# Optimization experiments

Measured on AMD Instinct MI355X. Metric: run time of the kernel, lower is better.

Reference implementation:

```python
import jax, jax.numpy as jnp
import numpy as np

HIDDEN = 1152
N_HEADS = 4
N_KV = 1
HEAD_DIM = 256
EPS = 1e-6
B, S = 4, 2048
ROPE_THETA = 1000000.0


def _rms_norm(x, w):
    # x: [..., D] float32; Gemma-style (1 + w) scale
    xf = x.astype(jnp.float32)
    inv = jax.lax.rsqrt(jnp.mean(xf * xf, axis=-1, keepdims=True) + EPS)
    return (xf * inv * (1.0 + w.astype(jnp.float32))).astype(x.dtype)


def _apply_rope(x, cos, sin):
    # x: [B, H, S, D]; cos/sin: [S, D/2]
    d2 = x.shape[-1] // 2
    x1, x2 = x[..., :d2], x[..., d2:]
    cos = cos[None, None, :, :]
    sin = sin[None, None, :, :]
    xr = x1 * cos - x2 * sin
    xi = x1 * sin + x2 * cos
    return jnp.concatenate([xr, xi], axis=-1).astype(x.dtype)


def setup_inputs() -> dict:
    key = jax.random.key(0)
    k_h, k_qkv, k_qn, k_kn, k_o = jax.random.split(key, 5)
    hidden_states = jax.random.normal(k_h, (B, S, HIDDEN), dtype=jnp.float32)
    # causal additive mask [1,1,S,S]
    neg = jnp.finfo(jnp.float32).min
    causal = jnp.tril(jnp.ones((S, S), dtype=bool))
    attention_mask = jnp.where(causal, 0.0, neg)[None, None, :, :].astype(jnp.float32)
    # RoPE tables (complex freqs_cis split into cos/sin)
    inv_freq = 1.0 / (ROPE_THETA ** (np.arange(0, HEAD_DIM, 2, dtype=np.float32) / HEAD_DIM))
    ang = np.arange(S, dtype=np.float32)[:, None] * inv_freq[None, :]
    freqs_cos = jnp.asarray(np.cos(ang))
    freqs_sin = jnp.asarray(np.sin(ang))
    qkv_out = (N_HEADS + 2 * N_KV) * HEAD_DIM
    scale = HIDDEN ** -0.5
    w_qkv = jax.random.normal(k_qkv, (HIDDEN, qkv_out), dtype=jnp.float32) * scale
    w_o = jax.random.normal(k_o, (N_HEADS * HEAD_DIM, HIDDEN), dtype=jnp.float32) * (N_HEADS * HEAD_DIM) ** -0.5
    q_norm_w = jax.random.normal(k_qn, (HEAD_DIM,), dtype=jnp.float32) * 0.02
    k_norm_w = jax.random.normal(k_kn, (HEAD_DIM,), dtype=jnp.float32) * 0.02
    return {
        "hidden_states": hidden_states,
        "attention_mask": attention_mask,
        "freqs_cos": freqs_cos,
        "freqs_sin": freqs_sin,
        "w_qkv": w_qkv,
        "q_norm_w": q_norm_w,
        "k_norm_w": k_norm_w,
        "w_o": w_o,
    }


def reference(hidden_states, attention_mask, freqs_cos, freqs_sin, w_qkv, q_norm_w, k_norm_w, w_o):
    b, s, _ = hidden_states.shape
    groups = N_HEADS // N_KV
    scaling = HEAD_DIM ** -0.5

    qkv = jnp.einsum("bsh,ho->bso", hidden_states, w_qkv)
    q_end = N_HEADS * HEAD_DIM
    k_end = q_end + N_KV * HEAD_DIM
    q = qkv[:, :, :q_end].reshape(b, s, N_HEADS, HEAD_DIM).transpose(0, 2, 1, 3)
    k = qkv[:, :, q_end:k_end].reshape(b, s, N_KV, HEAD_DIM).transpose(0, 2, 1, 3)
    v = qkv[:, :, k_end:].reshape(b, s, N_KV, HEAD_DIM).transpose(0, 2, 1, 3)

    q = _rms_norm(q, q_norm_w)
    k = _rms_norm(k, k_norm_w)

    q = _apply_rope(q, freqs_cos, freqs_sin)
    k = _apply_rope(k, freqs_cos, freqs_sin)

    if groups > 1:
        k = jnp.repeat(k, groups, axis=1)  # [B, H, S, D]
        v = jnp.repeat(v, groups, axis=1)

    scores = jnp.einsum("bhqd,bhkd->bhqk", q * scaling, k)
    scores = scores + attention_mask.astype(jnp.float32)
    probs = jax.nn.softmax(scores.astype(jnp.float32), axis=-1).astype(q.dtype)

    attn = jnp.einsum("bhqk,bhkd->bhqd", probs, v)
    attn = attn.transpose(0, 2, 1, 3).reshape(b, s, N_HEADS * HEAD_DIM)
    return jnp.einsum("bsf,fh->bsh", attn, w_o)
```

## Files before the change

kernel.cpp:

```cpp
#include <hip/hip_runtime.h>

typedef _Float16 f16;
typedef _Float16 f16x8 __attribute__((ext_vector_type(8)));
typedef _Float16 f16x4 __attribute__((ext_vector_type(4)));
typedef float f32x4 __attribute__((ext_vector_type(4)));

#define NH 4
#define HD 256
#define BB 4
#define SS 2048
#define HID 1152
#define QKV_N 1536
#define ODIM (NH * HD)

#define QKV16_OFF 0L
#define OBUF_OFF 0L
#define OPART_OFF 16777216L
#define ML_OFF 44040192L
#define QB_OFF 50331648L
#define KB_OFF 67108864L
#define VT_OFF 71303168L
#define WQKVT_OFF 75497472L
#define WOT_OFF 79036416L

#define GLL16(gp, lp)                                                      \
  __builtin_amdgcn_global_load_lds(                                       \
      (const __attribute__((address_space(1))) char*)(gp),                \
      (__attribute__((address_space(3))) char*)(lp), 16, 0, 0)

template <typename ST>
__global__ __launch_bounds__(256) void transpose_cvt(
    const ST* __restrict__ src, long src_ld, long src_bs,
    f16* __restrict__ dst, long dst_ld, long dst_bs) {
  __shared__ float tile[32][33];
  src += (long)blockIdx.z * src_bs;
  dst += (long)blockIdx.z * dst_bs;
  int r0 = blockIdx.y * 32, c0 = blockIdx.x * 32;
  int tc = threadIdx.x & 31, tr = threadIdx.x >> 5;
#pragma unroll
  for (int i = 0; i < 4; ++i)
    tile[tr + i * 8][tc] = (float)src[(long)(r0 + tr + i * 8) * src_ld + c0 + tc];
  __syncthreads();
#pragma unroll
  for (int i = 0; i < 4; ++i)
    dst[(long)(c0 + tr + i * 8) * dst_ld + r0 + tc] = (f16)tile[tc][tr + i * 8];
}

template <typename AT, typename CT>
__global__ __launch_bounds__(256, 3) void gemm_x(
    const AT* __restrict__ A, const f16* __restrict__ Bt,
    CT* __restrict__ C, int K, int N) {
  __shared__ f16 As[128][64];
  __shared__ f16 Bs[128][64];
  int tid = threadIdx.x, wave = tid >> 6, lane = tid & 63;
  int l16 = lane & 15, lhi = lane >> 4;
  int wm = (wave >> 1) * 64, wn = (wave & 1) * 64;
  long bm = (long)blockIdx.x * 128, bn = (long)blockIdx.y * 128;
  f32x4 acc[4][4] = {};

  int srow = wave * 32 + (lane >> 3), scol = (lane & 7) * 8;
  const f16* Bg = Bt + (bn + srow) * (long)K + scol;
  const f16* Agh = nullptr;
  const float* Agf = nullptr;
  int ar = tid >> 2, ac = (tid & 3) * 16;
  if constexpr (sizeof(AT) == 2)
    Agh = (const f16*)A + (bm + srow) * (long)K + scol;
  else
    Agf = (const float*)A + (bm + ar) * (long)K + ac;

  for (int k0 = 0; k0 < K; k0 += 64) {
    if constexpr (sizeof(AT) == 2) {
#pragma unroll
      for (int i = 0; i < 4; ++i)
        GLL16(Agh + k0 + (long)i * 8 * K, &As[wave * 32 + i * 8][0]);
    } else {
#pragma unroll
      for (int g = 0; g < 2; ++g) {
        const float* src = Agf + k0 + (long)g * 64 * K;
        float4 v0 = *(const float4*)(src + 0);
        float4 v1 = *(const float4*)(src + 4);
        float4 v2 = *(const float4*)(src + 8);
        float4 v3 = *(const float4*)(src + 12);
        f16x8 h0 = {(f16)v0.x, (f16)v0.y, (f16)v0.z, (f16)v0.w,
                    (f16)v1.x, (f16)v1.y, (f16)v1.z, (f16)v1.w};
        f16x8 h1 = {(f16)v2.x, (f16)v2.y, (f16)v2.z, (f16)v2.w,
                    (f16)v3.x, (f16)v3.y, (f16)v3.z, (f16)v3.w};
        *(f16x8*)&As[ar + 64 * g][ac] = h0;
        *(f16x8*)&As[ar + 64 * g][ac + 8] = h1;
      }
    }
#pragma unroll
    for (int i = 0; i < 4; ++i)
      GLL16(Bg + k0 + (long)i * 8 * K, &Bs[wave * 32 + i * 8][0]);
    __syncthreads();
#pragma unroll
    for (int kb = 0; kb < 2; ++kb) {
      f16x8 af[4], bf[4];
#pragma unroll
      for (int i = 0; i < 4; ++i)
        af[i] = *(const f16x8*)&As[wm + i * 16 + l16][kb * 32 + lhi * 8];
#pragma unroll
      for (int j = 0; j < 4; ++j)
        bf[j] = *(const f16x8*)&Bs[wn + j * 16 + l16][kb * 32 + lhi * 8];
#pragma unroll
      for (int i = 0; i < 4; ++i)
#pragma unroll
        for (int j = 0; j < 4; ++j)
          acc[i][j] =
              __builtin_amdgcn_mfma_f32_16x16x32_f16(bf[j], af[i], acc[i][j], 0, 0, 0);
    }
    __syncthreads();
  }

#pragma unroll
  for (int i = 0; i < 4; ++i) {
    long m = bm + wm + i * 16 + l16;
#pragma unroll
    for (int j = 0; j < 4; ++j) {
      long n = bn + wn + j * 16 + lhi * 4;
      if constexpr (sizeof(CT) == 2) {
        f16x4 h = {(f16)acc[i][j][0], (f16)acc[i][j][1], (f16)acc[i][j][2],
                   (f16)acc[i][j][3]};
        *(f16x4*)&C[m * N + n] = h;
      } else {
        *(f32x4*)&C[m * N + n] = acc[i][j];
      }
    }
  }
}

__device__ __forceinline__ void norm_rope_store(
    const f16* __restrict__ x, const float* __restrict__ w,
    const float* __restrict__ fc, const float* __restrict__ fs,
    f16* __restrict__ dst, float scale, int lane) {
  float x0 = (float)x[lane], x1 = (float)x[lane + 64];
  float x2 = (float)x[lane + 128], x3 = (float)x[lane + 192];
  float ss = x0 * x0 + x1 * x1 + x2 * x2 + x3 * x3;
#pragma unroll
  for (int m = 1; m < 64; m <<= 1) ss += __shfl_xor(ss, m, 64);
  float inv = rsqrtf(ss * (1.0f / 256.0f) + 1e-6f);
  x0 *= inv * (1.0f + w[lane]);
  x1 *= inv * (1.0f + w[lane + 64]);
  x2 *= inv * (1.0f + w[lane + 128]);
  x3 *= inv * (1.0f + w[lane + 192]);
  float c0 = fc[lane], s0 = fs[lane], c1 = fc[lane + 64], s1 = fs[lane + 64];
  dst[lane]       = (f16)((x0 * c0 - x2 * s0) * scale);
  dst[lane + 64]  = (f16)((x1 * c1 - x3 * s1) * scale);
  dst[lane + 128] = (f16)((x0 * s0 + x2 * c0) * scale);
  dst[lane + 192] = (f16)((x1 * s1 + x3 * c1) * scale);
}

__global__ __launch_bounds__(256) void qkv_post(
    const f16* __restrict__ qkv, const float* __restrict__ qnw,
    const float* __restrict__ knw, const float* __restrict__ fcos,
    const float* __restrict__ fsin, f16* __restrict__ Q, f16* __restrict__ Kb) {
  long row = blockIdx.x;
  int b = (int)(row >> 11), s = (int)(row & 2047);
  int wave = threadIdx.x >> 6, lane = threadIdx.x & 63;
  const f16* base = qkv + row * QKV_N;
  const float* fc = fcos + (long)s * 128;
  const float* fs = fsin + (long)s * 128;
  norm_rope_store(base + wave * HD, qnw, fc, fs,
                  Q + ((long)(b * NH + wave) * SS + s) * HD, 0.0625f, lane);
  if (wave == 0)
    norm_rope_store(base + NH * HD, knw, fc, fs, Kb + row * HD, 1.0f, lane);
}

__global__ __launch_bounds__(256, 4) void attn_fwd(
    const f16* __restrict__ Q, const f16* __restrict__ Kb,
    const f16* __restrict__ Vt, f16* __restrict__ O,
    f16* __restrict__ Opart, float2* __restrict__ ml) {
  __shared__ f16 Klds[32 * 256];
  __shared__ f16 Vlds[256 * 32];
  __shared__ f16 Plds[4][16][40];
  int it = blockIdx.x, h = blockIdx.y, b = blockIdx.z;
  int qb, t0, t1, slot = 0;
  bool split;
  if (it < 11) {
    qb = it; t0 = 0; t1 = 2 * qb + 2; split = false;
  } else {
    int j = it - 11, c, nch, lbase;
    if (j < 22) {
      qb = 11 + (j >> 1); c = j & 1; nch = 2; lbase = (qb - 11) * 2;
    } else {
      int jj = j - 22, q3 = jj / 3;
      qb = 22 + q3; c = jj - q3 * 3; nch = 3; lbase = 22 + q3 * 3;
    }
    int tiles = 2 * qb + 2;
    t0 = tiles * c / nch;
    t1 = tiles * (c + 1) / nch;
    split = true;
    slot = (b * NH + h) * 52 + lbase + c;
  }
  int tid = threadIdx.x, wave = tid >> 6, lane = tid & 63;
  int l16 = lane & 15, lhi = lane >> 4;
  int q0 = qb * 64 + wave * 16;

  const f16* Kg = Kb + (long)b * SS * HD;
  const f16* Vg = Vt + (long)b * HD * SS;

  f16x8 qf[8];
  const f16* Qbase = Q + ((long)(b * NH + h) * SS + q0 + l16) * HD + lhi * 8;
#pragma unroll
  for (int kb = 0; kb < 8; ++kb) qf[kb] = *(const f16x8*)(Qbase + kb * 32);

  f32x4 o[16] = {};
  float m_i = -1e30f, l_i = 0.f;

  int kr = tid >> 5, kc16 = (tid & 31) * 16;
  int rv = tid >> 2, vc16 = (tid & 3) * 16;
  char* kls = (char*)Klds;
  char* vls = (char*)Vlds;
  int kwsw = kc16 ^ (kr << 4);
  int vwsw = vc16 ^ ((rv & 3) << 4);
  const char* krd = kls + l16 * 512;
  int kswz = (l16 & 7) << 4;
  const char* vrd = vls + l16 * 64 + ((lhi * 16) ^ ((l16 & 3) << 4));

  for (int t = t0; t < t1; ++t) {
    long kv0 = (long)t * 32;
    __syncthreads();
#pragma unroll
    for (int i = 0; i < 4; ++i) {
      uint4 kval = *(const uint4*)((const char*)(Kg + (kv0 + kr + 8 * i) * HD) + kc16);
      *(uint4*)(kls + (kr + 8 * i) * 512 + kwsw) = kval;
    }
#pragma unroll
    for (int i = 0; i < 4; ++i) {
      uint4 vval = *(const uint4*)((const char*)(Vg + (long)(rv + 64 * i) * SS + kv0) + vc16);
      *(uint4*)(vls + (rv + 64 * i) * 64 + vwsw) = vval;
    }
    __syncthreads();

    f32x4 sc[2] = {};
    __builtin_amdgcn_s_setprio(1);
#pragma unroll
    for (int kb = 0; kb < 8; ++kb) {
#pragma unroll
      for (int cf = 0; cf < 2; ++cf) {
        f16x8 kf = *(const f16x8*)(krd + cf * 8192 + ((kb * 64 + lhi * 16) ^ kswz));
        sc[cf] = __builtin_amdgcn_mfma_f32_16x16x32_f16(kf, qf[kb], sc[cf], 0, 0, 0);
      }
    }
    __builtin_amdgcn_s_setprio(0);

    float p[8];
    float mx = -1e30f;
    int qrow = q0 + l16;
    if (t >= 2 * qb) {
#pragma unroll
      for (int cf = 0; cf < 2; ++cf)
#pragma unroll
        for (int r = 0; r < 4; ++r) {
          int kv = (int)kv0 + cf * 16 + lhi * 4 + r;
          float s = (kv <= qrow) ? sc[cf][r] : -1e30f;
          p[cf * 4 + r] = s;
          mx = fmaxf(mx, s);
        }
    } else {
#pragma unroll
      for (int i = 0; i < 8; ++i) {
        float s = sc[i >> 2][i & 3];
        p[i] = s;
        mx = fmaxf(mx, s);
      }
    }
    mx = fmaxf(mx, __shfl_xor(mx, 16));
    mx = fmaxf(mx, __shfl_xor(mx, 32));
    float mn = fmaxf(m_i, mx);
    float scl = __expf(m_i - mn);
    float rs = 0.f;
#pragma unroll
    for (int i = 0; i < 8; ++i) {
      p[i] = __expf(p[i] - mn);
      rs += p[i];
    }
    rs += __shfl_xor(rs, 16);
    rs += __shfl_xor(rs, 32);
    l_i = l_i * scl + rs;
    m_i = mn;

#pragma unroll
    for (int cf = 0; cf < 2; ++cf) {
      f16x4 hp = {(f16)p[cf * 4], (f16)p[cf * 4 + 1], (f16)p[cf * 4 + 2],
                  (f16)p[cf * 4 + 3]};
      *(f16x4*)&Plds[wave][l16][cf * 16 + lhi * 4] = hp;
    }

    float s0 = __shfl(scl, lhi * 4 + 0);
    float s1 = __shfl(scl, lhi * 4 + 1);
    float s2 = __shfl(scl, lhi * 4 + 2);
    float s3 = __shfl(scl, lhi * 4 + 3);
#pragma unroll
    for (int nf = 0; nf < 16; ++nf) {
      o[nf][0] *= s0;
      o[nf][1] *= s1;
      o[nf][2] *= s2;
      o[nf][3] *= s3;
    }

    f16x8 pa = *(const f16x8*)&Plds[wave][l16][lhi * 8];
    __builtin_amdgcn_s_setprio(1);
#pragma unroll
    for (int nf = 0; nf < 16; ++nf) {
      f16x8 vf = *(const f16x8*)(vrd + nf * 1024);
      o[nf] = __builtin_amdgcn_mfma_f32_16x16x32_f16(pa, vf, o[nf], 0, 0, 0);
    }
    __builtin_amdgcn_s_setprio(0);
  }

  float inv = 1.0f / l_i;
  float i0 = __shfl(inv, lhi * 4 + 0);
  float i1 = __shfl(inv, lhi * 4 + 1);
  float i2 = __shfl(inv, lhi * 4 + 2);
  float i3 = __shfl(inv, lhi * 4 + 3);
  float ir[4] = {i0, i1, i2, i3};
  if (!split) {
#pragma unroll
    for (int r = 0; r < 4; ++r) {
      long srow = q0 + lhi * 4 + r;
      f16* Orow = O + ((long)b * SS + srow) * ODIM + h * HD + l16;
#pragma unroll
      for (int nf = 0; nf < 16; ++nf) Orow[nf * 16] = (f16)(o[nf][r] * ir[r]);
    }
  } else {
#pragma unroll
    for (int r = 0; r < 4; ++r) {
      int rloc = wave * 16 + lhi * 4 + r;
      f16* Prow = Opart + ((long)slot * 64 + rloc) * HD + l16;
#pragma unroll
      for (int nf = 0; nf < 16; ++nf) Prow[nf * 16] = (f16)(o[nf][r] * ir[r]);
    }
    if (lane < 16) {
      float2 v; v.x = m_i; v.y = l_i;
      ml[(long)slot * 64 + wave * 16 + lane] = v;
    }
  }
}

__global__ __launch_bounds__(256) void attn_combine(
    const f16* __restrict__ Opart, const float2* __restrict__ ml,
    f16* __restrict__ O) {
  int x = blockIdx.x, h = blockIdx.y, b = blockIdx.z;
  int qb = 11 + x;
  int nch = (qb < 22) ? 2 : 3;
  int lbase = (qb < 22) ? (qb - 11) * 2 : 22 + (qb - 22) * 3;
  long slot0 = (long)(b * NH + h) * 52 + lbase;
  int tid = threadIdx.x;
  int r = tid >> 2, d0 = (tid & 3) * 64;
  float m[3], l[3], w[3];
  float M = -1e30f;
#pragma unroll
  for (int c = 0; c < 3; ++c)
    if (c < nch) {
      float2 v = ml[(slot0 + c) * 64 + r];
      m[c] = v.x; l[c] = v.y;
      M = fmaxf(M, v.x);
    }
  float sum = 0.f;
#pragma unroll
  for (int c = 0; c < 3; ++c)
    if (c < nch) { w[c] = l[c] * __expf(m[c] - M); sum += w[c]; }
  float inv = 1.0f / sum;
#pragma unroll
  for (int c = 0; c < 3; ++c)
    if (c < nch) w[c] *= inv;
  f16* Orow = O + ((long)b * SS + qb * 64 + r) * ODIM + h * HD + d0;
#pragma unroll
  for (int i = 0; i < 8; ++i) {
    float acc[8] = {};
#pragma unroll
    for (int c = 0; c < 3; ++c)
      if (c < nch) {
        f16x8 xv = *(const f16x8*)(Opart + ((slot0 + c) * 64 + r) * HD + d0 + i * 8);
#pragma unroll
        for (int j = 0; j < 8; ++j) acc[j] += w[c] * (float)xv[j];
      }
    f16x8 z;
#pragma unroll
    for (int j = 0; j < 8; ++j) z[j] = (f16)acc[j];
    *(f16x8*)(Orow + i * 8) = z;
  }
}

extern "C" void kernel_launch(void* const* d_in, const int* in_sizes, int n_in,
                              void* d_out, int out_size, void* d_ws, size_t ws_size,
                              hipStream_t stream) {
  const float* hidden = (const float*)d_in[0];
  const float* fcos = (const float*)d_in[2];
  const float* fsin = (const float*)d_in[3];
  const float* wqkv = (const float*)d_in[4];
  const float* qnw = (const float*)d_in[5];
  const float* knw = (const float*)d_in[6];
  const float* wo = (const float*)d_in[7];
  float* out = (float*)d_out;

  char* ws = (char*)d_ws;
  f16* qkv16 = (f16*)(ws + QKV16_OFF);
  f16* Obuf = (f16*)(ws + OBUF_OFF);
  f16* Opart = (f16*)(ws + OPART_OFF);
  float2* ml = (float2*)(ws + ML_OFF);
  f16* Qb = (f16*)(ws + QB_OFF);
  f16* Kb = (f16*)(ws + KB_OFF);
  f16* Vt = (f16*)(ws + VT_OFF);
  f16* wqkvt = (f16*)(ws + WQKVT_OFF);
  f16* wot = (f16*)(ws + WOT_OFF);

  transpose_cvt<float><<<dim3(QKV_N / 32, HID / 32, 1), 256, 0, stream>>>(
      wqkv, QKV_N, 0, wqkvt, HID, 0);
  transpose_cvt<float><<<dim3(HID / 32, ODIM / 32, 1), 256, 0, stream>>>(
      wo, HID, 0, wot, ODIM, 0);

  gemm_x<float, f16><<<dim3(BB * SS / 128, QKV_N / 128), 256, 0, stream>>>(
      hidden, wqkvt, qkv16, HID, QKV_N);

  qkv_post<<<dim3(BB * SS), 256, 0, stream>>>(qkv16, qnw, knw, fcos, fsin, Qb, Kb);

  transpose_cvt<f16><<<dim3(HD / 32, SS / 32, BB), 256, 0, stream>>>(
      qkv16 + 1280, QKV_N, (long)SS * QKV_N, Vt, SS, (long)HD * SS);

  attn_fwd<<<dim3(63, NH, BB), 256, 0, stream>>>(Qb, Kb, Vt, Obuf, Opart, ml);
  attn_combine<<<dim3(21, NH, BB), 256, 0, stream>>>(Opart, ml, Obuf);

  gemm_x<f16, float><<<dim3(BB * SS / 128, HID / 128), 256, 0, stream>>>(
      Obuf, wot, out, ODIM, HID);
}
```

Baseline: 279.5 us.

## Pre-convert hidden states to f16 and remap attention blocks by XCD

Adds a separate kernel that converts the fp32 hidden states to f16 once, so the QKV GEMM can load A tiles with direct global-to-LDS loads instead of loading fp32 in registers and converting. This removes the redundant fp32 loads and conversions repeated across the N-dimension blocks, at the cost of an extra pass over memory and another launch. It also flattens the attention grid to 1D and remaps block IDs so that blocks sharing a batch land on the same XCD, aiming for better L2 reuse of K/V, with some blocks exiting early as padding.

Measured after the change: 240.6 us. 1.16x faster.

```diff
diff --git a/kernel.cpp b/kernel.cpp
--- a/kernel.cpp
+++ b/kernel.cpp
@@ -14,6 +14,7 @@
 #define ODIM (NH * HD)
 
 #define QKV16_OFF 0L
+#define HID16_OFF 25165824L
 #define OBUF_OFF 0L
 #define OPART_OFF 16777216L
 #define ML_OFF 44040192L
@@ -27,6 +28,19 @@
   __builtin_amdgcn_global_load_lds(                                       \
       (const __attribute__((address_space(1))) char*)(gp),                \
       (__attribute__((address_space(3))) char*)(lp), 16, 0, 0)
+
+__global__ __launch_bounds__(256) void cvt_f32_to_f16(
+    const float* __restrict__ s, f16* __restrict__ d, long n) {
+  long i = ((long)blockIdx.x * 256 + threadIdx.x) * 8;
+  long stride = (long)gridDim.x * 256 * 8;
+  for (; i < n; i += stride) {
+    float4 a = *(const float4*)(s + i);
+    float4 b = *(const float4*)(s + i + 4);
+    f16x8 h = {(f16)a.x, (f16)a.y, (f16)a.z, (f16)a.w,
+               (f16)b.x, (f16)b.y, (f16)b.z, (f16)b.w};
+    *(f16x8*)(d + i) = h;
+  }
+}
 
 template <typename ST>
 __global__ __launch_bounds__(256) void transpose_cvt(
@@ -46,9 +60,9 @@
     dst[(long)(c0 + tr + i * 8) * dst_ld + r0 + tc] = (f16)tile[tc][tr + i * 8];
 }
 
-template <typename AT, typename CT>
-__global__ __launch_bounds__(256, 3) void gemm_x(
-    const AT* __restrict__ A, const f16* __restrict__ Bt,
+template <typename CT>
+__global__ __launch_bounds__(256, 3) void gemm_f16(
+    const f16* __restrict__ A, const f16* __restrict__ Bt,
     CT* __restrict__ C, int K, int N) {
   __shared__ f16 As[128][64];
   __shared__ f16 Bs[128][64];
@@ -58,37 +72,15 @@
   long bm = (long)blockIdx.x * 128, bn = (long)blockIdx.y * 128;
   f32x4 acc[4][4] = {};
 
-  int srow = wave * 32 + (lane >> 3), scol = (lane & 7) * 8;
+  int srow = wave * 32 + (lane >> 3);
+  int scol = (lane & 7) * 8;
+  const f16* Ag = A + (bm + srow) * (long)K + scol;
   const f16* Bg = Bt + (bn + srow) * (long)K + scol;
-  const f16* Agh = nullptr;
-  const float* Agf = nullptr;
-  int ar = tid >> 2, ac = (tid & 3) * 16;
-  if constexpr (sizeof(AT) == 2)
-    Agh = (const f16*)A + (bm + srow) * (long)K + scol;
-  else
-    Agf = (const float*)A + (bm + ar) * (long)K + ac;
 
   for (int k0 = 0; k0 < K; k0 += 64) {
-    if constexpr (sizeof(AT) == 2) {
-#pragma unroll
-      for (int i = 0; i < 4; ++i)
-        GLL16(Agh + k0 + (long)i * 8 * K, &As[wave * 32 + i * 8][0]);
-    } else {
-#pragma unroll
-      for (int g = 0; g < 2; ++g) {
-        const float* src = Agf + k0 + (long)g * 64 * K;
-        float4 v0 = *(const float4*)(src + 0);
-        float4 v1 = *(const float4*)(src + 4);
-        float4 v2 = *(const float4*)(src + 8);
-        float4 v3 = *(const float4*)(src + 12);
-        f16x8 h0 = {(f16)v0.x, (f16)v0.y, (f16)v0.z, (f16)v0.w,
-                    (f16)v1.x, (f16)v1.y, (f16)v1.z, (f16)v1.w};
-        f16x8 h1 = {(f16)v2.x, (f16)v2.y, (f16)v2.z, (f16)v2.w,
-                    (f16)v3.x, (f16)v3.y, (f16)v3.z, (f16)v3.w};
-        *(f16x8*)&As[ar + 64 * g][ac] = h0;
-        *(f16x8*)&As[ar + 64 * g][ac + 8] = h1;
-      }
-    }
+#pragma unroll
+    for (int i = 0; i < 4; ++i)
+      GLL16(Ag + k0 + (long)i * 8 * K, &As[wave * 32 + i * 8][0]);
 #pragma unroll
     for (int i = 0; i < 4; ++i)
       GLL16(Bg + k0 + (long)i * 8 * K, &Bs[wave * 32 + i * 8][0]);
@@ -173,7 +165,13 @@
   __shared__ f16 Klds[32 * 256];
   __shared__ f16 Vlds[256 * 32];
   __shared__ f16 Plds[4][16][40];
-  int it = blockIdx.x, h = blockIdx.y, b = blockIdx.z;
+  int bid = blockIdx.x;
+  int xcd = bid & 7, slotid = bid >> 3;
+  int b = xcd >> 1, par = xcd & 1;
+  int h = slotid >> 5, ithalf = slotid & 31;
+  int it = ithalf * 2 + par;
+  if (it >= 63) return;
+
   int qb, t0, t1, slot = 0;
   bool split;
   if (it < 11) {
@@ -397,6 +395,7 @@
 
   char* ws = (char*)d_ws;
   f16* qkv16 = (f16*)(ws + QKV16_OFF);
+  f16* hid16 = (f16*)(ws + HID16_OFF);
   f16* Obuf = (f16*)(ws + OBUF_OFF);
   f16* Opart = (f16*)(ws + OPART_OFF);
   float2* ml = (float2*)(ws + ML_OFF);
@@ -406,22 +405,24 @@
   f16* wqkvt = (f16*)(ws + WQKVT_OFF);
   f16* wot = (f16*)(ws + WOT_OFF);
 
+  cvt_f32_to_f16<<<2048, 256, 0, stream>>>(hidden, hid16, (long)BB * SS * HID);
+
   transpose_cvt<float><<<dim3(QKV_N / 32, HID / 32, 1), 256, 0, stream>>>(
       wqkv, QKV_N, 0, wqkvt, HID, 0);
   transpose_cvt<float><<<dim3(HID / 32, ODIM / 32, 1), 256, 0, stream>>>(
       wo, HID, 0, wot, ODIM, 0);
 
-  gemm_x<float, f16><<<dim3(BB * SS / 128, QKV_N / 128), 256, 0, stream>>>(
-      hidden, wqkvt, qkv16, HID, QKV_N);
+  gemm_f16<f16><<<dim3(BB * SS / 128, QKV_N / 128), 256, 0, stream>>>(
+      hid16, wqkvt, qkv16, HID, QKV_N);
 
   qkv_post<<<dim3(BB * SS), 256, 0, stream>>>(qkv16, qnw, knw, fcos, fsin, Qb, Kb);
 
   transpose_cvt<f16><<<dim3(HD / 32, SS / 32, BB), 256, 0, stream>>>(
       qkv16 + 1280, QKV_N, (long)SS * QKV_N, Vt, SS, (long)HD * SS);
 
-  attn_fwd<<<dim3(63, NH, BB), 256, 0, stream>>>(Qb, Kb, Vt, Obuf, Opart, ml);
+  attn_fwd<<<dim3(1024), 256, 0, stream>>>(Qb, Kb, Vt, Obuf, Opart, ml);
   attn_combine<<<dim3(21, NH, BB), 256, 0, stream>>>(Opart, ml, Obuf);
 
-  gemm_x<f16, float><<<dim3(BB * SS / 128, HID / 128), 256, 0, stream>>>(
+  gemm_f16<float><<<dim3(BB * SS / 128, HID / 128), 256, 0, stream>>>(
       Obuf, wot, out, ODIM, HID);
 }
```
